# Kernel optimization log

Hardware: AMD Instinct MI355X
Metric: run time of the kernel (lower is better)

Reference implementation:

```python
import jax, jax.numpy as jnp
import numpy as np

NUM_HEADS = 16


def rotary_pos_emb(x):
    # x: [b, h, s, d] with interleaved rotary pairs (d even)
    d, s = x.shape[-1], x.shape[-2]
    ts = jnp.arange(0, d, 2, dtype=jnp.float32)
    inv_freqs = 10000.0 ** (-ts / d)                      # [d/2]
    grid = jnp.arange(s, dtype=jnp.float32)[:, None] * inv_freqs[None, :]  # [s, d/2]
    sin = jnp.repeat(jnp.sin(grid), 2, axis=-1)           # [s, d]
    cos = jnp.repeat(jnp.cos(grid), 2, axis=-1)           # [s, d]
    x1, x2 = x[..., ::2], x[..., 1::2]
    xs = jnp.stack([-x2, x1], axis=-1).reshape(x.shape)   # rotate pairs
    return x * cos + xs * sin


def setup_inputs() -> dict:
    key = jax.random.key(0)
    ks = jax.random.split(key, 6)
    b, l, d = 2, 2048, 1024
    x = jax.random.normal(ks[0], (b, l, d), dtype=jnp.float32)
    # additive causal mask: 0 on/below diag, large negative above
    causal = jnp.tril(jnp.ones((l, l), dtype=bool))
    mask = jnp.where(causal, 0.0, -1e9).astype(jnp.float32)[None, None]  # [1,1,l,l]
    s = 0.01  # VarianceScaling(0.01)-ish small init
    Wq = jax.random.normal(ks[1], (d, d), dtype=jnp.float32) * s
    Wk = jax.random.normal(ks[2], (d, d), dtype=jnp.float32) * s
    Wv = jax.random.normal(ks[3], (d, d), dtype=jnp.float32) * s
    Wo = jax.random.normal(ks[4], (d, d), dtype=jnp.float32) * s
    return {"x": x, "mask": mask, "Wq": Wq, "Wk": Wk, "Wv": Wv, "Wo": Wo}


def reference(x, mask, Wq, Wk, Wv, Wo):
    b, l, d = x.shape
    h = NUM_HEADS
    k_sz = d // h
    split = lambda t: t.reshape(b, l, h, k_sz).transpose(0, 2, 1, 3)  # b h l k
    # NOTE: original scales q by 1/sqrt(model_dim) (not key_size), before RoPE
    q = split(x @ Wq / jnp.sqrt(jnp.float32(d)))
    q = rotary_pos_emb(q)
    k = rotary_pos_emb(split(x @ Wk))
    v = split(x @ Wv)
    logits = jnp.einsum('bhik,bhjk->bhij', q, k) + mask   # [b,h,l,l]
    a = jax.nn.softmax(logits, axis=-1)
    y = jnp.einsum('bhij,bhjv->bhiv', a, v)               # [b,h,l,k]
    y = y.transpose(0, 2, 1, 3).reshape(b, l, d)
    return y @ Wo
```

## Files before the change

kernel.cpp:

```cpp
#include <hip/hip_runtime.h>
#include <math.h>

#define L 2048
#define D 1024
#define H 16
#define KS 64
#define BBATCH 2

typedef float f32x4 __attribute__((ext_vector_type(4)));
typedef short s16x8 __attribute__((ext_vector_type(8)));

__device__ __forceinline__ ushort f2bf(float f) {
    union { float f; unsigned u; } v; v.f = f;
    unsigned lsb = (v.u >> 16) & 1u;
    v.u += 0x7fffu + lsb;
    return (ushort)(v.u >> 16);
}

__device__ __forceinline__ unsigned fbits(float f) {
    union { float f; unsigned u; } v; v.f = f; return v.u;
}

__device__ __forceinline__ void gl_lds16(const ushort* g, ushort* l) {
    __builtin_amdgcn_global_load_lds(
        (const __attribute__((address_space(1))) unsigned int*)g,
        (__attribute__((address_space(3))) unsigned int*)l, 16, 0, 0);
}

__global__ __launch_bounds__(256)
void prep(const float* __restrict__ x,
          const float* __restrict__ W0, const float* __restrict__ W1,
          const float* __restrict__ W2, const float* __restrict__ W3,
          ushort* __restrict__ xb, ushort* __restrict__ Wt,
          float2* __restrict__ tab)
{
    __shared__ float T[32][33];
    const int bid = blockIdx.x;
    const int tid = threadIdx.x;
    if (bid < 4096) {
        const int i = bid * 1024 + tid * 4;
        const float4 v = *(const float4*)&x[i];
        ushort4 p = make_ushort4(f2bf(v.x), f2bf(v.y), f2bf(v.z), f2bf(v.w));
        *(ushort4*)&xb[i] = p;
    } else if (bid < 8192) {
        const int t = bid - 4096;
        const int z = t >> 10;
        const float* W = (z == 0) ? W0 : (z == 1) ? W1 : (z == 2) ? W2 : W3;
        ushort* out = Wt + (size_t)z * D * D;
        const int r0 = ((t >> 5) & 31) * 32, c0 = (t & 31) * 32;
        const int tr = tid >> 3, tc = (tid & 7) * 4;
        const float4 v = *(const float4*)&W[(size_t)(r0 + tr) * D + c0 + tc];
        T[tr][tc + 0] = v.x; T[tr][tc + 1] = v.y;
        T[tr][tc + 2] = v.z; T[tr][tc + 3] = v.w;
        __syncthreads();
        ushort4 p = make_ushort4(f2bf(T[tc + 0][tr]), f2bf(T[tc + 1][tr]),
                                 f2bf(T[tc + 2][tr]), f2bf(T[tc + 3][tr]));
        *(ushort4*)&out[(size_t)(c0 + tr) * D + r0 + tc] = p;
    } else {
        const int idx = (bid - 8192) * 256 + tid;
        const int dd2 = idx >> 11, s = idx & 2047;
        const float inv = __expf(-(float)(2 * dd2) * (9.210340371976184f / 64.0f));
        float sn, cs;
        sincosf((float)s * inv, &sn, &cs);
        tab[idx] = make_float2(cs, sn);
    }
}

__global__ __launch_bounds__(512, 2)
void qkv_gemm(const ushort* __restrict__ A, const ushort* __restrict__ B,
              const float2* __restrict__ tab,
              ushort* __restrict__ Qo, ushort* __restrict__ Ko,
              ushort* __restrict__ Vto)
{
    __shared__ __align__(16) ushort smem[65536];
    const int tid  = threadIdx.x;
    const int wv   = tid >> 6, lane = tid & 63;
    const int i16  = lane & 15, quad = lane >> 4;
    const int wr   = wv >> 2, wc = wv & 3;

    int bid = blockIdx.y * 16 + blockIdx.x;
    bid = (bid & 7) * 24 + (bid >> 3);
    const int by = bid % 12, bx = bid / 12;
    const int m0 = by * 256, n0 = bx * 256;

    const int c0 = tid, c1 = tid + 512;
    const size_t sA0 = (size_t)(m0 + (c0 >> 2)) * D + (((c0 & 3) * 8) ^ (((c0 >> 4) & 3) << 3));
    const size_t sA1 = (size_t)(m0 + (c1 >> 2)) * D + (((c1 & 3) * 8) ^ (((c1 >> 4) & 3) << 3));
    const size_t sB0 = (size_t)(n0 + (c0 >> 2)) * D + (((c0 & 3) * 8) ^ (((c0 >> 4) & 3) << 3));
    const size_t sB1 = (size_t)(n0 + (c1 >> 2)) * D + (((c1 & 3) * 8) ^ (((c1 >> 4) & 3) << 3));
    const int l0 = c0 * 8, l1 = c1 * 8;

    f32x4 acc[8][4];
    #pragma unroll
    for (int i = 0; i < 8; ++i)
        #pragma unroll
        for (int j = 0; j < 4; ++j) acc[i][j] = (f32x4){0.f, 0.f, 0.f, 0.f};

#define STAGE_A(kt) do { ushort* As_ = smem + ((kt) & 3) * 16384;             \
        gl_lds16(A + sA0 + (size_t)(kt) * 32, As_ + l0);                      \
        gl_lds16(A + sA1 + (size_t)(kt) * 32, As_ + l1); } while (0)
#define STAGE_B(kt) do { ushort* Bs_ = smem + ((kt) & 3) * 16384 + 8192;      \
        gl_lds16(B + sB0 + (size_t)(kt) * 32, Bs_ + l0);                      \
        gl_lds16(B + sB1 + (size_t)(kt) * 32, Bs_ + l1); } while (0)

    STAGE_A(0); STAGE_B(0);
    STAGE_A(1); STAGE_B(1);
    STAGE_A(2); STAGE_B(2);
    asm volatile("s_waitcnt vmcnt(8)" ::: "memory");
    __builtin_amdgcn_s_barrier();

    #pragma unroll 1
    for (int kt = 0; kt < 32; ++kt) {
        const ushort* As = smem + (kt & 3) * 16384;
        const ushort* Bs = As + 8192;
        s16x8 afr[4], bfr[4];

        #pragma unroll
        for (int mf = 0; mf < 4; ++mf) {
            int ad = (wr * 128 + mf * 16 + i16) * 64 + quad * 16;
            ad ^= ((ad >> 8) & 3) << 4;
            afr[mf] = *(const s16x8*)((const char*)As + ad);
        }
        #pragma unroll
        for (int nf = 0; nf < 4; ++nf) {
            int ad = (wc * 64 + nf * 16 + i16) * 64 + quad * 16;
            ad ^= ((ad >> 8) & 3) << 4;
            bfr[nf] = *(const s16x8*)((const char*)Bs + ad);
        }
        if (kt < 29) STAGE_A(kt + 3);
        __builtin_amdgcn_s_barrier();
        asm volatile("s_waitcnt lgkmcnt(0)" ::: "memory");
        __builtin_amdgcn_sched_barrier(0);
        __builtin_amdgcn_s_setprio(1);
        #pragma unroll
        for (int mf = 0; mf < 4; ++mf)
            #pragma unroll
            for (int nf = 0; nf < 4; ++nf)
                acc[mf][nf] = __builtin_amdgcn_mfma_f32_16x16x32_bf16(
                    afr[mf], bfr[nf], acc[mf][nf], 0, 0, 0);
        __builtin_amdgcn_s_setprio(0);
        __builtin_amdgcn_s_barrier();

        #pragma unroll
        for (int mf = 0; mf < 4; ++mf) {
            int ad = (wr * 128 + (mf + 4) * 16 + i16) * 64 + quad * 16;
            ad ^= ((ad >> 8) & 3) << 4;
            afr[mf] = *(const s16x8*)((const char*)As + ad);
        }
        if (kt < 29) STAGE_B(kt + 3);
        __builtin_amdgcn_s_barrier();
        asm volatile("s_waitcnt lgkmcnt(0)" ::: "memory");
        __builtin_amdgcn_sched_barrier(0);
        __builtin_amdgcn_s_setprio(1);
        #pragma unroll
        for (int mf = 0; mf < 4; ++mf)
            #pragma unroll
            for (int nf = 0; nf < 4; ++nf)
                acc[mf + 4][nf] = __builtin_amdgcn_mfma_f32_16x16x32_bf16(
                    afr[mf], bfr[nf], acc[mf + 4][nf], 0, 0, 0);
        __builtin_amdgcn_s_setprio(0);

        if (kt <= 28)      { asm volatile("s_waitcnt vmcnt(8)" ::: "memory"); }
        else if (kt == 29) { asm volatile("s_waitcnt vmcnt(4)" ::: "memory"); }
        else if (kt == 30) { asm volatile("s_waitcnt vmcnt(0)" ::: "memory"); }
        __builtin_amdgcn_s_barrier();
    }
#undef STAGE_A
#undef STAGE_B

    if (m0 < 2048) {
        const bool isQ = (m0 < 1024);
        ushort* out = isQ ? Qo : Ko;
        const int mb2 = isQ ? m0 : (m0 - 1024);
        #pragma unroll
        for (int mf = 0; mf < 8; ++mf)
            #pragma unroll
            for (int nf = 0; nf < 4; ++nf) {
                const int token = n0 + wc * 64 + nf * 16 + i16;
                const int b = token >> 11, s = token & 2047;
                const int dim = mb2 + wr * 128 + mf * 16 + quad * 4;
                const int hh = dim >> 6, dd = dim & 63;
                ushort4 p;
                #pragma unroll
                for (int pr = 0; pr < 2; ++pr) {
                    float e = acc[mf][nf][2 * pr];
                    float o = acc[mf][nf][2 * pr + 1];
                    if (isQ) { e *= 0.03125f; o *= 0.03125f; }
                    const float2 cssn = tab[(size_t)((dd >> 1) + pr) * 2048 + s];
                    const float ne = e * cssn.x - o * cssn.y;
                    const float no = o * cssn.x + e * cssn.y;
                    if (pr == 0) { p.x = f2bf(ne); p.y = f2bf(no); }
                    else         { p.z = f2bf(ne); p.w = f2bf(no); }
                }
                *(ushort4*)&out[((size_t)(b * H + hh) * L + s) * KS + dd] = p;
            }
    } else {
        ushort* T = smem + wv * 4608;
        const int tbase = n0 + wc * 64;
        #pragma unroll
        for (int hh2 = 0; hh2 < 2; ++hh2) {
            const int vbase = (m0 - 2048) + wr * 128 + hh2 * 64;
            #pragma unroll
            for (int mf = 0; mf < 4; ++mf)
                #pragma unroll
                for (int nf = 0; nf < 4; ++nf) {
                    #pragma unroll
                    for (int r = 0; r < 4; ++r)
                        T[(mf * 16 + quad * 4 + r) * 72 + nf * 16 + i16] =
                            f2bf(acc[hh2 * 4 + mf][nf][r]);
                }
            __builtin_amdgcn_s_waitcnt(0);
            const int tl0 = (lane & 7) * 8;
            #pragma unroll
            for (int c = 0; c < 8; ++c) {
                const int vl = c * 8 + (lane >> 3);
                const s16x8 val = *(const s16x8*)&T[vl * 72 + tl0];
                const int vdim = vbase + vl;
                const int hh = vdim >> 6, dd = vdim & 63;
                const int token0 = tbase + tl0;
                const int b = token0 >> 11, s0 = token0 & 2047;
                *(s16x8*)&Vto[((size_t)(b * H + hh) * KS + dd) * L + s0] = val;
            }
            if (hh2 == 0) __builtin_amdgcn_s_waitcnt(0);
        }
    }
}

__global__ __launch_bounds__(256)
void oproj_gemm(const ushort* __restrict__ A, const ushort* __restrict__ B,
                float* __restrict__ out)
{
    __shared__ __align__(16) ushort smem[12288];
    const int tid  = threadIdx.x;
    const int wv   = tid >> 6, lane = tid & 63;
    const int i16  = lane & 15, quad = lane >> 4;
    const int wr   = wv >> 1, wc = wv & 1;
    const int m0   = blockIdx.y * 128;
    const int n0   = blockIdx.x * 64;

    const int cA0 = wv * 64 + lane, cA1 = 256 + wv * 64 + lane;

    f32x4 acc[4][2];
    #pragma unroll
    for (int i = 0; i < 4; ++i)
        #pragma unroll
        for (int j = 0; j < 2; ++j) acc[i][j] = (f32x4){0.f, 0.f, 0.f, 0.f};

    {
        ushort* As = smem;
        ushort* Bs = smem + 4096;
        gl_lds16(A + (size_t)(m0 + (cA0 >> 2)) * D + (cA0 & 3) * 8, As + (size_t)(wv * 64) * 8);
        gl_lds16(A + (size_t)(m0 + (cA1 >> 2)) * D + (cA1 & 3) * 8, As + (size_t)(256 + wv * 64) * 8);
        gl_lds16(B + (size_t)(n0 + (cA0 >> 2)) * D + (cA0 & 3) * 8, Bs + (size_t)(wv * 64) * 8);
    }
    __syncthreads();

    for (int it = 0; it < 32; ++it) {
        const int cur = it & 1;
        if (it + 1 < 32) {
            const int kn = (it + 1) * 32;
            ushort* As = smem + (cur ^ 1) * 6144;
            ushort* Bs = As + 4096;
            gl_lds16(A + (size_t)(m0 + (cA0 >> 2)) * D + kn + (cA0 & 3) * 8, As + (size_t)(wv * 64) * 8);
            gl_lds16(A + (size_t)(m0 + (cA1 >> 2)) * D + kn + (cA1 & 3) * 8, As + (size_t)(256 + wv * 64) * 8);
            gl_lds16(B + (size_t)(n0 + (cA0 >> 2)) * D + kn + (cA0 & 3) * 8, Bs + (size_t)(wv * 64) * 8);
        }
        const ushort* As = smem + cur * 6144;
        const ushort* Bs = As + 4096;
        s16x8 af[4], bf[2];
        #pragma unroll
        for (int mt = 0; mt < 4; ++mt)
            af[mt] = *(const s16x8*)&As[(wr * 64 + mt * 16 + i16) * 32 + quad * 8];
        #pragma unroll
        for (int nt = 0; nt < 2; ++nt)
            bf[nt] = *(const s16x8*)&Bs[(wc * 32 + nt * 16 + i16) * 32 + quad * 8];
        #pragma unroll
        for (int mt = 0; mt < 4; ++mt)
            #pragma unroll
            for (int nt = 0; nt < 2; ++nt)
                acc[mt][nt] = __builtin_amdgcn_mfma_f32_16x16x32_bf16(
                    af[mt], bf[nt], acc[mt][nt], 0, 0, 0);
        __syncthreads();
    }

    #pragma unroll
    for (int mt = 0; mt < 4; ++mt)
        #pragma unroll
        for (int nt = 0; nt < 2; ++nt) {
            const int od = n0 + wc * 32 + nt * 16 + i16;
            const int tk = m0 + wr * 64 + mt * 16 + quad * 4;
            #pragma unroll
            for (int r = 0; r < 4; ++r)
                out[(size_t)(tk + r) * D + od] = acc[mt][nt][r];
        }
}

__global__ __launch_bounds__(512)
void attn_mfma(const ushort* __restrict__ Q, const ushort* __restrict__ K,
               const ushort* __restrict__ Vt, ushort* __restrict__ Yb)
{
    const int bh   = blockIdx.y;
    const int qa   = blockIdx.x;
    const int qb   = 31 - qa;
    const int tid  = threadIdx.x;
    const int wave = tid >> 6, lane = tid & 63;
    const int half = wave >> 2, wv4 = wave & 3;
    const int i16  = lane & 15, quad = lane >> 4;
    const int qt   = half ? qb : qa;
    const int r0   = qt * 64 + wv4 * 16;
    const int row  = r0 + i16;

    __shared__ ushort Ks[2][64 * 72];
    __shared__ ushort Vs[2][64 * 72];
    __shared__ ushort Ps[8][16 * 72];

    const ushort* Qb = Q  + (size_t)bh * L * KS;
    const ushort* Kb = K  + (size_t)bh * L * KS;
    const ushort* Vb = Vt + (size_t)bh * KS * L;

    const s16x8 qf0 = *(const s16x8*)(Qb + (size_t)row * KS + quad * 8);
    const s16x8 qf1 = *(const s16x8*)(Qb + (size_t)row * KS + 32 + quad * 8);

    const int sr = tid >> 3, sseg = (tid & 7) * 8;
    s16x8 kpre = *(const s16x8*)(Kb + (size_t)sr * KS + sseg);
    s16x8 vpre = *(const s16x8*)(Vb + (size_t)sr * L + sseg);
    *(s16x8*)&Ks[0][sr * 72 + sseg] = kpre;
    *(s16x8*)&Vs[0][sr * 72 + sseg] = vpre;
    __syncthreads();

    f32x4 O0 = {0.f,0.f,0.f,0.f}, O1 = O0, O2 = O0, O3 = O0;
    float psum = 0.0f;

    for (int jt = 0; jt <= qb; ++jt) {
        const int cur = jt & 1;
        const bool has_next = (jt < qb);

        if (has_next) {
            const int j0n = (jt + 1) * 64;
            kpre = *(const s16x8*)(Kb + (size_t)(j0n + sr) * KS + sseg);
            vpre = *(const s16x8*)(Vb + (size_t)sr * L + j0n + sseg);
        }

        if (jt <= qt) {
            const int j0 = jt * 64;
            const ushort* Ksb = &Ks[cur][0];
            const ushort* Vsb = &Vs[cur][0];
            f32x4 st[4];
            #pragma unroll
            for (int nt = 0; nt < 4; ++nt) {
                const s16x8 kf0 = *(const s16x8*)&Ksb[(nt * 16 + i16) * 72 + quad * 8];
                const s16x8 kf1 = *(const s16x8*)&Ksb[(nt * 16 + i16) * 72 + 32 + quad * 8];
                f32x4 c = {0.f,0.f,0.f,0.f};
                c = __builtin_amdgcn_mfma_f32_16x16x32_bf16(kf0, qf0, c, 0, 0, 0);
                c = __builtin_amdgcn_mfma_f32_16x16x32_bf16(kf1, qf1, c, 0, 0, 0);
                st[nt] = c;
            }
            if (jt == qt) {
                #pragma unroll
                for (int nt = 0; nt < 4; ++nt)
                    #pragma unroll
                    for (int rg = 0; rg < 4; ++rg) {
                        const int j = j0 + nt * 16 + quad * 4 + rg;
                        if (j > row) st[nt][rg] = -1e30f;
                    }
            }
            float pv[4][4];
            #pragma unroll
            for (int nt = 0; nt < 4; ++nt)
                #pragma unroll
                for (int rg = 0; rg < 4; ++rg) {
                    pv[nt][rg] = __expf(st[nt][rg]);
                    psum += pv[nt][rg];
                }
            ushort* P2 = &Ps[wave][0];
            #pragma unroll
            for (int nt = 0; nt < 4; ++nt) {
                uint2 pk;
                pk.x = __builtin_amdgcn_perm(fbits(pv[nt][1]), fbits(pv[nt][0]), 0x07060302u);
                pk.y = __builtin_amdgcn_perm(fbits(pv[nt][3]), fbits(pv[nt][2]), 0x07060302u);
                *(uint2*)(P2 + i16 * 72 + nt * 16 + quad * 4) = pk;
            }
            const s16x8 pf0 = *(const s16x8*)(P2 + i16 * 72 + quad * 8);
            const s16x8 pf1 = *(const s16x8*)(P2 + i16 * 72 + 32 + quad * 8);
            s16x8 v0, v1;
            v0 = *(const s16x8*)&Vsb[(0 * 16 + i16) * 72 + quad * 8];
            v1 = *(const s16x8*)&Vsb[(0 * 16 + i16) * 72 + 32 + quad * 8];
            O0 = __builtin_amdgcn_mfma_f32_16x16x32_bf16(v0, pf0, O0, 0, 0, 0);
            O0 = __builtin_amdgcn_mfma_f32_16x16x32_bf16(v1, pf1, O0, 0, 0, 0);
            v0 = *(const s16x8*)&Vsb[(1 * 16 + i16) * 72 + quad * 8];
            v1 = *(const s16x8*)&Vsb[(1 * 16 + i16) * 72 + 32 + quad * 8];
            O1 = __builtin_amdgcn_mfma_f32_16x16x32_bf16(v0, pf0, O1, 0, 0, 0);
            O1 = __builtin_amdgcn_mfma_f32_16x16x32_bf16(v1, pf1, O1, 0, 0, 0);
            v0 = *(const s16x8*)&Vsb[(2 * 16 + i16) * 72 + quad * 8];
            v1 = *(const s16x8*)&Vsb[(2 * 16 + i16) * 72 + 32 + quad * 8];
            O2 = __builtin_amdgcn_mfma_f32_16x16x32_bf16(v0, pf0, O2, 0, 0, 0);
            O2 = __builtin_amdgcn_mfma_f32_16x16x32_bf16(v1, pf1, O2, 0, 0, 0);
            v0 = *(const s16x8*)&Vsb[(3 * 16 + i16) * 72 + quad * 8];
            v1 = *(const s16x8*)&Vsb[(3 * 16 + i16) * 72 + 32 + quad * 8];
            O3 = __builtin_amdgcn_mfma_f32_16x16x32_bf16(v0, pf0, O3, 0, 0, 0);
            O3 = __builtin_amdgcn_mfma_f32_16x16x32_bf16(v1, pf1, O3, 0, 0, 0);
        }

        if (has_next) {
            *(s16x8*)&Ks[cur ^ 1][sr * 72 + sseg] = kpre;
            *(s16x8*)&Vs[cur ^ 1][sr * 72 + sseg] = vpre;
            __syncthreads();
        }
    }

    psum += __shfl_xor(psum, 16);
    psum += __shfl_xor(psum, 32);
    const float inv_l = __builtin_amdgcn_rcpf(psum);
    const int b = bh >> 4, hh = bh & 15;
    ushort* Yp = Yb + ((size_t)(b * L + row)) * D + hh * KS + quad * 4;
    f32x4 r;
    r = O0 * inv_l; *(ushort4*)(Yp +  0) = make_ushort4(f2bf(r[0]),f2bf(r[1]),f2bf(r[2]),f2bf(r[3]));
    r = O1 * inv_l; *(ushort4*)(Yp + 16) = make_ushort4(f2bf(r[0]),f2bf(r[1]),f2bf(r[2]),f2bf(r[3]));
    r = O2 * inv_l; *(ushort4*)(Yp + 32) = make_ushort4(f2bf(r[0]),f2bf(r[1]),f2bf(r[2]),f2bf(r[3]));
    r = O3 * inv_l; *(ushort4*)(Yp + 48) = make_ushort4(f2bf(r[0]),f2bf(r[1]),f2bf(r[2]),f2bf(r[3]));
}

extern "C" void kernel_launch(void* const* d_in, const int* in_sizes, int n_in,
                              void* d_out, int out_size, void* d_ws, size_t ws_size,
                              hipStream_t stream)
{
    const float* x  = (const float*)d_in[0];
    const float* Wq = (const float*)d_in[2];
    const float* Wk = (const float*)d_in[3];
    const float* Wv = (const float*)d_in[4];
    const float* Wo = (const float*)d_in[5];

    const size_t NTOK = (size_t)BBATCH * L;
    const size_t SZ   = NTOK * D;
    ushort* xb  = (ushort*)d_ws;
    ushort* Wt  = xb + SZ;
    ushort* Qb  = Wt + 4 * (size_t)D * D;
    ushort* Kb  = Qb + SZ;
    ushort* Vtb = Kb + SZ;
    ushort* Yb  = Vtb + SZ;
    float2* tab = (float2*)Yb;

    prep<<<dim3(8448), dim3(256), 0, stream>>>(x, Wq, Wk, Wv, Wo, xb, Wt, tab);

    qkv_gemm<<<dim3(16, 12), dim3(512), 0, stream>>>(Wt, xb, tab, Qb, Kb, Vtb);

    attn_mfma<<<dim3(16, 32), dim3(512), 0, stream>>>(Qb, Kb, Vtb, Yb);

    oproj_gemm<<<dim3(16, 32), dim3(256), 0, stream>>>(Yb, Wt + 3 * (size_t)D * D,
                                                       (float*)d_out);
}
```

Before: 193.6 us.

## Deepen oproj GEMM pipeline with larger tiles and split attention blocks

```diff
diff --git a/kernel.cpp b/kernel.cpp
--- a/kernel.cpp
+++ b/kernel.cpp
@@ -230,89 +230,103 @@
 void oproj_gemm(const ushort* __restrict__ A, const ushort* __restrict__ B,
                 float* __restrict__ out)
 {
-    __shared__ __align__(16) ushort smem[12288];
+    __shared__ __align__(16) ushort smem[32768];
     const int tid  = threadIdx.x;
     const int wv   = tid >> 6, lane = tid & 63;
     const int i16  = lane & 15, quad = lane >> 4;
     const int wr   = wv >> 1, wc = wv & 1;
-    const int m0   = blockIdx.y * 128;
-    const int n0   = blockIdx.x * 64;
-
-    const int cA0 = wv * 64 + lane, cA1 = 256 + wv * 64 + lane;
-
-    f32x4 acc[4][2];
+
+    const int bid = blockIdx.y * 8 + blockIdx.x;
+    const int bx  = bid & 7, by = bid >> 3;
+    const int m0  = by * 128, n0 = bx * 128;
+
+    const int c0 = tid, c1 = tid + 256;
+    const size_t sA0 = (size_t)(m0 + (c0 >> 2)) * D + (((c0 & 3) * 8) ^ (((c0 >> 4) & 3) << 3));
+    const size_t sA1 = (size_t)(m0 + (c1 >> 2)) * D + (((c1 & 3) * 8) ^ (((c1 >> 4) & 3) << 3));
+    const size_t sB0 = (size_t)(n0 + (c0 >> 2)) * D + (((c0 & 3) * 8) ^ (((c0 >> 4) & 3) << 3));
+    const size_t sB1 = (size_t)(n0 + (c1 >> 2)) * D + (((c1 & 3) * 8) ^ (((c1 >> 4) & 3) << 3));
+    const int l0 = c0 * 8, l1 = c1 * 8;
+
+    f32x4 acc[4][4];
     #pragma unroll
     for (int i = 0; i < 4; ++i)
         #pragma unroll
-        for (int j = 0; j < 2; ++j) acc[i][j] = (f32x4){0.f, 0.f, 0.f, 0.f};
-
-    {
-        ushort* As = smem;
-        ushort* Bs = smem + 4096;
-        gl_lds16(A + (size_t)(m0 + (cA0 >> 2)) * D + (cA0 & 3) * 8, As + (size_t)(wv * 64) * 8);
-        gl_lds16(A + (size_t)(m0 + (cA1 >> 2)) * D + (cA1 & 3) * 8, As + (size_t)(256 + wv * 64) * 8);
-        gl_lds16(B + (size_t)(n0 + (cA0 >> 2)) * D + (cA0 & 3) * 8, Bs + (size_t)(wv * 64) * 8);
+        for (int j = 0; j < 4; ++j) acc[i][j] = (f32x4){0.f, 0.f, 0.f, 0.f};
+
+#define OSTAGE(kt) do { ushort* As_ = smem + ((kt) & 3) * 8192;               \
+        gl_lds16(A + sA0 + (size_t)(kt) * 32, As_ + l0);                      \
+        gl_lds16(A + sA1 + (size_t)(kt) * 32, As_ + l1);                      \
+        gl_lds16(B + sB0 + (size_t)(kt) * 32, As_ + 4096 + l0);               \
+        gl_lds16(B + sB1 + (size_t)(kt) * 32, As_ + 4096 + l1); } while (0)
+
+    OSTAGE(0); OSTAGE(1); OSTAGE(2);
+    asm volatile("s_waitcnt vmcnt(8)" ::: "memory");
+    __builtin_amdgcn_s_barrier();
+
+    #pragma unroll 1
+    for (int kt = 0; kt < 32; ++kt) {
+        const ushort* As = smem + (kt & 3) * 8192;
+        const ushort* Bs = As + 4096;
+        s16x8 afr[4], bfr[4];
+        #pragma unroll
+        for (int mf = 0; mf < 4; ++mf) {
+            int ad = (wr * 64 + mf * 16 + i16) * 64 + quad * 16;
+            ad ^= ((ad >> 8) & 3) << 4;
+            afr[mf] = *(const s16x8*)((const char*)As + ad);
+        }
+        #pragma unroll
+        for (int nf = 0; nf < 4; ++nf) {
+            int ad = (wc * 64 + nf * 16 + i16) * 64 + quad * 16;
+            ad ^= ((ad >> 8) & 3) << 4;
+            bfr[nf] = *(const s16x8*)((const char*)Bs + ad);
+        }
+        if (kt < 29) OSTAGE(kt + 3);
+        __builtin_amdgcn_s_barrier();
+        asm volatile("s_waitcnt lgkmcnt(0)" ::: "memory");
+        __builtin_amdgcn_sched_barrier(0);
+        __builtin_amdgcn_s_setprio(1);
+        #pragma unroll
+        for (int mf = 0; mf < 4; ++mf)
+            #pragma unroll
+            for (int nf = 0; nf < 4; ++nf)
+                acc[mf][nf] = __builtin_amdgcn_mfma_f32_16x16x32_bf16(
+                    afr[mf], bfr[nf], acc[mf][nf], 0, 0, 0);
+        __builtin_amdgcn_s_setprio(0);
+
+        if (kt <= 28)      { asm volatile("s_waitcnt vmcnt(8)" ::: "memory"); }
+        else if (kt == 29) { asm volatile("s_waitcnt vmcnt(4)" ::: "memory"); }
+        else if (kt == 30) { asm volatile("s_waitcnt vmcnt(0)" ::: "memory"); }
+        __builtin_amdgcn_s_barrier();
     }
-    __syncthreads();
-
-    for (int it = 0; it < 32; ++it) {
-        const int cur = it & 1;
-        if (it + 1 < 32) {
-            const int kn = (it + 1) * 32;
-            ushort* As = smem + (cur ^ 1) * 6144;
-            ushort* Bs = As + 4096;
-            gl_lds16(A + (size_t)(m0 + (cA0 >> 2)) * D + kn + (cA0 & 3) * 8, As + (size_t)(wv * 64) * 8);
-            gl_lds16(A + (size_t)(m0 + (cA1 >> 2)) * D + kn + (cA1 & 3) * 8, As + (size_t)(256 + wv * 64) * 8);
-            gl_lds16(B + (size_t)(n0 + (cA0 >> 2)) * D + kn + (cA0 & 3) * 8, Bs + (size_t)(wv * 64) * 8);
-        }
-        const ushort* As = smem + cur * 6144;
-        const ushort* Bs = As + 4096;
-        s16x8 af[4], bf[2];
-        #pragma unroll
-        for (int mt = 0; mt < 4; ++mt)
-            af[mt] = *(const s16x8*)&As[(wr * 64 + mt * 16 + i16) * 32 + quad * 8];
-        #pragma unroll
-        for (int nt = 0; nt < 2; ++nt)
-            bf[nt] = *(const s16x8*)&Bs[(wc * 32 + nt * 16 + i16) * 32 + quad * 8];
-        #pragma unroll
-        for (int mt = 0; mt < 4; ++mt)
-            #pragma unroll
-            for (int nt = 0; nt < 2; ++nt)
-                acc[mt][nt] = __builtin_amdgcn_mfma_f32_16x16x32_bf16(
-                    af[mt], bf[nt], acc[mt][nt], 0, 0, 0);
-        __syncthreads();
-    }
+#undef OSTAGE
 
     #pragma unroll
-    for (int mt = 0; mt < 4; ++mt)
-        #pragma unroll
-        for (int nt = 0; nt < 2; ++nt) {
-            const int od = n0 + wc * 32 + nt * 16 + i16;
-            const int tk = m0 + wr * 64 + mt * 16 + quad * 4;
+    for (int mf = 0; mf < 4; ++mf)
+        #pragma unroll
+        for (int nf = 0; nf < 4; ++nf) {
+            const int od = n0 + wc * 64 + nf * 16 + i16;
+            const int tk = m0 + wr * 64 + mf * 16 + quad * 4;
             #pragma unroll
             for (int r = 0; r < 4; ++r)
-                out[(size_t)(tk + r) * D + od] = acc[mt][nt][r];
-        }
-}
-
-__global__ __launch_bounds__(512)
+                out[(size_t)(tk + r) * D + od] = acc[mf][nf][r];
+        }
+}
+
+__global__ __launch_bounds__(256)
 void attn_mfma(const ushort* __restrict__ Q, const ushort* __restrict__ K,
                const ushort* __restrict__ Vt, ushort* __restrict__ Yb)
 {
     const int bh   = blockIdx.y;
-    const int qa   = blockIdx.x;
-    const int qb   = 31 - qa;
+    const int qt   = 31 - blockIdx.x;
     const int tid  = threadIdx.x;
     const int wave = tid >> 6, lane = tid & 63;
-    const int half = wave >> 2, wv4 = wave & 3;
     const int i16  = lane & 15, quad = lane >> 4;
-    const int qt   = half ? qb : qa;
-    const int r0   = qt * 64 + wv4 * 16;
+    const int r0   = qt * 64 + wave * 16;
     const int row  = r0 + i16;
 
     __shared__ ushort Ks[2][64 * 72];
     __shared__ ushort Vs[2][64 * 72];
-    __shared__ ushort Ps[8][16 * 72];
+    __shared__ ushort Ps[4][16 * 72];
 
     const ushort* Qb = Q  + (size_t)bh * L * KS;
     const ushort* Kb = K  + (size_t)bh * L * KS;
@@ -321,27 +335,33 @@
     const s16x8 qf0 = *(const s16x8*)(Qb + (size_t)row * KS + quad * 8);
     const s16x8 qf1 = *(const s16x8*)(Qb + (size_t)row * KS + 32 + quad * 8);
 
-    const int sr = tid >> 3, sseg = (tid & 7) * 8;
-    s16x8 kpre = *(const s16x8*)(Kb + (size_t)sr * KS + sseg);
-    s16x8 vpre = *(const s16x8*)(Vb + (size_t)sr * L + sseg);
-    *(s16x8*)&Ks[0][sr * 72 + sseg] = kpre;
-    *(s16x8*)&Vs[0][sr * 72 + sseg] = vpre;
+    const int sr = tid >> 2, ss = (tid & 3) * 16;
+    s16x8 kp0 = *(const s16x8*)(Kb + (size_t)sr * KS + ss);
+    s16x8 kp1 = *(const s16x8*)(Kb + (size_t)sr * KS + ss + 8);
+    s16x8 vp0 = *(const s16x8*)(Vb + (size_t)sr * L + ss);
+    s16x8 vp1 = *(const s16x8*)(Vb + (size_t)sr * L + ss + 8);
+    *(s16x8*)&Ks[0][sr * 72 + ss]     = kp0;
+    *(s16x8*)&Ks[0][sr * 72 + ss + 8] = kp1;
+    *(s16x8*)&Vs[0][sr * 72 + ss]     = vp0;
+    *(s16x8*)&Vs[0][sr * 72 + ss + 8] = vp1;
     __syncthreads();
 
     f32x4 O0 = {0.f,0.f,0.f,0.f}, O1 = O0, O2 = O0, O3 = O0;
     float psum = 0.0f;
 
-    for (int jt = 0; jt <= qb; ++jt) {
+    for (int jt = 0; jt <= qt; ++jt) {
         const int cur = jt & 1;
-        const bool has_next = (jt < qb);
+        const bool has_next = (jt < qt);
 
         if (has_next) {
             const int j0n = (jt + 1) * 64;
-            kpre = *(const s16x8*)(Kb + (size_t)(j0n + sr) * KS + sseg);
-            vpre = *(const s16x8*)(Vb + (size_t)sr * L + j0n + sseg);
-        }
-
-        if (jt <= qt) {
+            kp0 = *(const s16x8*)(Kb + (size_t)(j0n + sr) * KS + ss);
+            kp1 = *(const s16x8*)(Kb + (size_t)(j0n + sr) * KS + ss + 8);
+            vp0 = *(const s16x8*)(Vb + (size_t)sr * L + j0n + ss);
+            vp1 = *(const s16x8*)(Vb + (size_t)sr * L + j0n + ss + 8);
+        }
+
+        {
             const int j0 = jt * 64;
             const ushort* Ksb = &Ks[cur][0];
             const ushort* Vsb = &Vs[cur][0];
@@ -402,8 +422,10 @@
         }
 
         if (has_next) {
-            *(s16x8*)&Ks[cur ^ 1][sr * 72 + sseg] = kpre;
-            *(s16x8*)&Vs[cur ^ 1][sr * 72 + sseg] = vpre;
+            *(s16x8*)&Ks[cur ^ 1][sr * 72 + ss]     = kp0;
+            *(s16x8*)&Ks[cur ^ 1][sr * 72 + ss + 8] = kp1;
+            *(s16x8*)&Vs[cur ^ 1][sr * 72 + ss]     = vp0;
+            *(s16x8*)&Vs[cur ^ 1][sr * 72 + ss + 8] = vp1;
             __syncthreads();
         }
     }
@@ -444,8 +466,8 @@
 
     qkv_gemm<<<dim3(16, 12), dim3(512), 0, stream>>>(Wt, xb, tab, Qb, Kb, Vtb);
 
-    attn_mfma<<<dim3(16, 32), dim3(512), 0, stream>>>(Qb, Kb, Vtb, Yb);
-
-    oproj_gemm<<<dim3(16, 32), dim3(256), 0, stream>>>(Yb, Wt + 3 * (size_t)D * D,
-                                                       (float*)d_out);
-}
+    attn_mfma<<<dim3(32, 32), dim3(256), 0, stream>>>(Qb, Kb, Vtb, Yb);
+
+    oproj_gemm<<<dim3(8, 32), dim3(256), 0, stream>>>(Yb, Wt + 3 * (size_t)D * D,
+                                                      (float*)d_out);
+}
```

Measured after the change: 226.2 us. +16.9%, slower.
